# Performance work log

Measured on AMD Instinct MI355X. Metric: run time of the kernel, lower is better.

The kernel has to match this reference:

```python
import jax, jax.numpy as jnp
import numpy as np

N_LIC, N_EMP, N_CON = 40000, 80000, 60000
D_LIC, D_EMP, D_CON = 256, 128, 192
H = 256
E_P, E_Q = 1280000, 640000


def setup_inputs() -> dict:
    key = jax.random.key(0)
    ks = jax.random.split(key, 13)
    s = 0.05
    return {
        "x_lic": jax.random.normal(ks[0], (N_LIC, D_LIC), jnp.float32),
        "x_emp": jax.random.normal(ks[1], (N_EMP, D_EMP), jnp.float32),
        "x_con": jax.random.normal(ks[2], (N_CON, D_CON), jnp.float32),
        "Wl_p": jax.random.normal(ks[3], (D_EMP, H), jnp.float32) * s,
        "Wr_p": jax.random.normal(ks[4], (D_LIC, H), jnp.float32) * s,
        "b_p": jax.random.normal(ks[5], (H,), jnp.float32) * s,
        "Wl_q": jax.random.normal(ks[6], (D_CON, H), jnp.float32) * s,
        "Wr_q": jax.random.normal(ks[7], (D_LIC, H), jnp.float32) * s,
        "b_q": jax.random.normal(ks[8], (H,), jnp.float32) * s,
        "ei_p_src": jax.random.randint(ks[9], (E_P,), 0, N_EMP, jnp.int64),
        "ei_p_dst": jax.random.randint(ks[10], (E_P,), 0, N_LIC, jnp.int64),
        "ei_q_src": jax.random.randint(ks[11], (E_Q,), 0, N_CON, jnp.int64),
        "ei_q_dst": jax.random.randint(ks[12], (E_Q,), 0, N_LIC, jnp.int64),
    }


def _sage_conv(x_src, x_dst, src, dst, Wl, Wr, b):
    """PyG SAGEConv (mean aggr): lin_l(mean_neighbors) + lin_r(x_dst) + bias."""
    n_dst = x_dst.shape[0]
    # gather src features per edge, scatter-sum to dst nodes
    agg = jax.ops.segment_sum(x_src[src], dst, num_segments=n_dst)  # [n_dst, d_src]
    deg = jax.ops.segment_sum(jnp.ones(src.shape, x_src.dtype), dst, num_segments=n_dst)
    agg = agg / jnp.maximum(deg, 1.0)[:, None]  # zero-degree nodes -> 0 (PyG semantics)
    return agg @ Wl + x_dst @ Wr + b


def reference(x_lic, x_emp, x_con, Wl_p, Wr_p, b_p, Wl_q, Wr_q, b_q,
              ei_p_src, ei_p_dst, ei_q_src, ei_q_dst):
    # to_hetero dispatch: two relations target 'licitacion'; aggr='mean' across relations.
    out_p = _sage_conv(x_emp, x_lic, ei_p_src, ei_p_dst, Wl_p, Wr_p, b_p)  # empresa->licitacion
    out_q = _sage_conv(x_con, x_lic, ei_q_src, ei_q_dst, Wl_q, Wr_q, b_q)  # contrato->licitacion
    # forward returns x_dict['licitacion'] after relu; other dst types are dead code.
    return jax.nn.relu(0.5 * (out_p + out_q))
```

## Files before the change

### kernel.cpp

```cpp
#include <hip/hip_runtime.h>

#define N_LIC 40000
#define N_EMP 80000
#define N_CON 60000
#define D_EMP 128
#define D_CON 192
#define HDIM  256
#define E_P   1280000
#define E_Q   640000
#define E_T   (E_P + E_Q)

#define NSEG  64
#define SEGW  (2 * NSEG)
#define SUBR  (N_LIC / NSEG)

#define OFF_AGGP   0
#define OFF_STG    OFF_AGGP
#define OFF_XE     (OFF_AGGP + 2560000)
#define OFF_AGGQ   OFF_XE
#define OFF_XC     (OFF_XE + 5120000)
#define OFF_BPK    (OFF_XC + 5760000)
#define OFF_BIAS   (OFF_BPK + 73728)
#define OFF_CNT    (OFF_BIAS + 256)
#define OFF_SEGT   (OFF_CNT + 2 * N_LIC)
#define OFF_SEGB   (OFF_SEGT + 128)
#define OFF_SEGC   (OFF_SEGB + 128)
#define OFF_OFFP   (OFF_SEGC + 128)
#define OFF_OFFQ   (OFF_OFFP + N_LIC)
#define OFF_SRTP   (OFF_OFFQ + N_LIC)
#define OFF_SRTQ   (OFF_SRTP + E_P)

typedef short bf16x8 __attribute__((ext_vector_type(8)));
typedef float f32x4 __attribute__((ext_vector_type(4)));

__device__ __forceinline__ ushort f2bf(float f) {
    union { float f; uint u; } v; v.f = f;
    return (ushort)((v.u + 0x7fffu + ((v.u >> 16) & 1u)) >> 16);
}

__device__ __forceinline__ void acc2(uint u, float& lo, float& hi) {
    union { uint u; float f; } a, b;
    a.u = u << 16;
    b.u = u & 0xffff0000u;
    lo += a.f; hi += b.f;
}

__device__ __forceinline__ uint packbf(float lo, float hi) {
    return (uint)f2bf(lo) | ((uint)f2bf(hi) << 16);
}

__global__ void prep_kernel(const float* __restrict__ Wlp, const float* __restrict__ Wlq,
                            const float* __restrict__ Wrp, const float* __restrict__ Wrq,
                            const float* __restrict__ bp, const float* __restrict__ bq,
                            ushort* __restrict__ Bpk, float* __restrict__ bias) {
    int tid = blockIdx.x * 256 + threadIdx.x;
    if (tid < 256 * 576) {
        int n = tid / 576, k = tid - n * 576;
        float v;
        if (k < 128)      v = Wlp[k * 256 + n];
        else if (k < 320) v = Wlq[(k - 128) * 256 + n];
        else              v = Wrp[(k - 320) * 256 + n] + Wrq[(k - 320) * 256 + n];
        Bpk[tid] = f2bf(v);
    } else if (tid < 256 * 576 + 256) {
        int j = tid - 256 * 576;
        bias[j] = bp[j] + bq[j];
    }
}

#define C_XE (N_EMP * 128 / 4)
#define C_XC (N_CON * 192 / 4)
__global__ void convert2_kernel(const float* __restrict__ xemp, const float* __restrict__ xcon,
                                ushort* __restrict__ xe, ushort* __restrict__ xc) {
    int tid = blockIdx.x * 256 + threadIdx.x;
    const float* src; ushort* dst; int i;
    if (tid < C_XE) { src = xemp; dst = xe; i = tid; }
    else            { src = xcon; dst = xc; i = tid - C_XE; }
    float4 v = ((const float4*)src)[i];
    uint2 o;
    o.x = packbf(v.x, v.y);
    o.y = packbf(v.z, v.w);
    ((uint2*)dst)[i] = o;
}

__global__ __launch_bounds__(256) void precount_kernel(const int* __restrict__ dp,
                                                       const int* __restrict__ dq,
                                                       int* __restrict__ segtot) {
    __shared__ int lc[SEGW];
    int t = threadIdx.x;
    if (t < SEGW) lc[t] = 0;
    __syncthreads();
    int base = blockIdx.x * 2048 + t;
    #pragma unroll
    for (int i = 0; i < 8; i++) {
        int e = base + i * 256;
        if (e < E_T) {
            int d, rel;
            if (e < E_P) { d = __builtin_nontemporal_load(&dp[e]); rel = 0; }
            else         { d = __builtin_nontemporal_load(&dq[e - E_P]); rel = 1; }
            atomicAdd(&lc[rel * NSEG + d / SUBR], 1);
        }
    }
    __syncthreads();
    if (t < SEGW && lc[t] > 0) atomicAdd(&segtot[t], lc[t]);
}

__global__ void segbase_kernel(const int* __restrict__ segtot,
                               int* __restrict__ segbase, int* __restrict__ segcur) {
    if (threadIdx.x == 0) {
        int run = 0;
        for (int i = 0; i < SEGW; i++) {
            segbase[i] = run; segcur[i] = run;
            run += segtot[i];
        }
    }
}

__global__ __launch_bounds__(256) void partition_kernel(const int* __restrict__ sp,
                                                        const int* __restrict__ dp,
                                                        const int* __restrict__ sq,
                                                        const int* __restrict__ dq,
                                                        int* __restrict__ segcur,
                                                        uint* __restrict__ stg) {
    __shared__ int lc[SEGW], inc[SEGW], lb[SEGW], gb[SEGW];
    __shared__ uint srtd[2048];
    __shared__ uchar sid[2048];
    int t = threadIdx.x;
    if (t < SEGW) lc[t] = 0;
    __syncthreads();
    int seg[8], lo[8]; uint pk[8];
    int base = blockIdx.x * 2048 + t;
    #pragma unroll
    for (int i = 0; i < 8; i++) {
        int e = base + i * 256;
        seg[i] = -1;
        if (e < E_T) {
            int d, s, rel;
            if (e < E_P) {
                d = __builtin_nontemporal_load(&dp[e]);
                s = __builtin_nontemporal_load(&sp[e]); rel = 0;
            } else {
                int eq = e - E_P;
                d = __builtin_nontemporal_load(&dq[eq]);
                s = __builtin_nontemporal_load(&sq[eq]); rel = 1;
            }
            int sl = d / SUBR;
            int dl = d - sl * SUBR;
            seg[i] = rel * NSEG + sl;
            pk[i] = ((uint)dl << 17) | (uint)s;
            lo[i] = atomicAdd(&lc[seg[i]], 1);
        }
    }
    __syncthreads();
    if (t < SEGW) inc[t] = lc[t];
    __syncthreads();
    #pragma unroll
    for (int off = 1; off < SEGW; off <<= 1) {
        int v = (t >= off && t < SEGW) ? inc[t - off] : 0;
        __syncthreads();
        if (t < SEGW) inc[t] += v;
        __syncthreads();
    }
    if (t < SEGW) {
        lb[t] = inc[t] - lc[t];
        gb[t] = lc[t] > 0 ? atomicAdd(&segcur[t], lc[t]) : 0;
    }
    __syncthreads();
    #pragma unroll
    for (int i = 0; i < 8; i++) {
        if (seg[i] >= 0) {
            int p = lb[seg[i]] + lo[i];
            srtd[p] = pk[i];
            sid[p] = (uchar)seg[i];
        }
    }
    __syncthreads();
    int tot = inc[SEGW - 1];
    for (int p = t; p < tot; p += 256) {
        int s = sid[p];
        stg[gb[s] + (p - lb[s])] = srtd[p];
    }
}

#define LCAP 22528
__global__ __launch_bounds__(1024) void sort_kernel(const int* __restrict__ segbase,
                                                    const int* __restrict__ segcur,
                                                    const uint* __restrict__ stg,
                                                    int* __restrict__ srtp, int* __restrict__ srtq,
                                                    int* __restrict__ offp, int* __restrict__ offq,
                                                    int* __restrict__ cnt) {
    __shared__ int lcnt[SUBR], lcur[SUBR];
    __shared__ int sc[640];
    __shared__ uint buf[LCAP];
    int s = blockIdx.x;
    int rel = s >> 6;
    int beg = segbase[s], end = segcur[s];
    int t = threadIdx.x;
    if (t < SUBR) { lcnt[t] = 0; lcur[t] = 0; }
    __syncthreads();
    for (int idx = beg + t; idx < end; idx += 1024)
        atomicAdd(&lcnt[stg[idx] >> 17], 1);
    __syncthreads();
    if (t < 640) sc[t] = (t < SUBR) ? lcnt[t] : 0;
    __syncthreads();
    #pragma unroll
    for (int off = 1; off < 640; off <<= 1) {
        int v = (t >= off && t < 640) ? sc[t - off] : 0;
        __syncthreads();
        if (t < 640) sc[t] += v;
        __syncthreads();
    }
    int rb = (rel == 0) ? beg : beg - E_P;
    int* srt = (rel == 0) ? srtp : srtq;
    for (int idx = beg + t; idx < end; idx += 1024) {
        uint p = stg[idx];
        int dl = (int)(p >> 17);
        int pos = sc[dl] - lcnt[dl] + atomicAdd(&lcur[dl], 1);
        uint sv = p & 0x1FFFFu;
        if (pos < LCAP) buf[pos] = sv;
        else srt[rb + pos] = (int)sv;
    }
    __syncthreads();
    int n = end - beg;
    int m = n < LCAP ? n : LCAP;
    for (int p = t; p < m; p += 1024) srt[rb + p] = (int)buf[p];
    int dbase = (s & (NSEG - 1)) * SUBR;
    int* offs = (rel == 0) ? offp : offq;
    int* cn = (rel == 0) ? cnt : cnt + N_LIC;
    if (t < SUBR) {
        offs[dbase + t] = rb + sc[t] - lcnt[t];
        cn[dbase + t] = lcnt[t];
    }
}

__global__ __launch_bounds__(256) void aggP_kernel(const ushort* __restrict__ xe,
                                                   const int* __restrict__ offs,
                                                   const int* __restrict__ cnt,
                                                   const int* __restrict__ sorted,
                                                   ushort* __restrict__ agg) {
    int g = blockIdx.x * 16 + (threadIdx.x >> 4);
    int c = threadIdx.x & 15;
    int beg = offs[g], deg = cnt[g], end = beg + deg;
    float a0=0,a1=0,a2=0,a3=0,a4=0,a5=0,a6=0,a7=0;
    for (int eb = beg; eb < end; eb += 16) {
        int n = end - eb; if (n > 16) n = 16;
        int my = (c < n) ? sorted[eb + c] : 0;
        for (int j = 0; j < n; j++) {
            int s = __shfl(my, j, 16);
            uint4 v = *(const uint4*)(xe + (size_t)s * D_EMP + c * 8);
            acc2(v.x, a0, a1); acc2(v.y, a2, a3);
            acc2(v.z, a4, a5); acc2(v.w, a6, a7);
        }
    }
    float inv = 1.0f / fmaxf((float)deg, 1.0f);
    uint4 o;
    o.x = packbf(a0 * inv, a1 * inv);
    o.y = packbf(a2 * inv, a3 * inv);
    o.z = packbf(a4 * inv, a5 * inv);
    o.w = packbf(a6 * inv, a7 * inv);
    *(uint4*)(agg + (size_t)g * D_EMP + c * 8) = o;
}

__global__ __launch_bounds__(256) void aggQ_kernel(const ushort* __restrict__ xc,
                                                   const int* __restrict__ offs,
                                                   const int* __restrict__ cnt,
                                                   const int* __restrict__ sorted,
                                                   ushort* __restrict__ agg) {
    int g = blockIdx.x * 16 + (threadIdx.x >> 4);
    int c = threadIdx.x & 15;
    int beg = offs[g], deg = cnt[g], end = beg + deg;
    float a0=0,a1=0,a2=0,a3=0,a4=0,a5=0,a6=0,a7=0,a8=0,a9=0,a10=0,a11=0;
    for (int eb = beg; eb < end; eb += 16) {
        int n = end - eb; if (n > 16) n = 16;
        int my = (c < n) ? sorted[eb + c] : 0;
        for (int j = 0; j < n; j++) {
            int s = __shfl(my, j, 16);
            const ushort* row = xc + (size_t)s * D_CON + c * 12;
            uint2 v0 = *(const uint2*)(row + 0);
            uint2 v1 = *(const uint2*)(row + 4);
            uint2 v2 = *(const uint2*)(row + 8);
            acc2(v0.x, a0, a1);  acc2(v0.y, a2, a3);
            acc2(v1.x, a4, a5);  acc2(v1.y, a6, a7);
            acc2(v2.x, a8, a9);  acc2(v2.y, a10, a11);
        }
    }
    float inv = 1.0f / fmaxf((float)deg, 1.0f);
    ushort* o = agg + (size_t)g * D_CON + c * 12;
    uint2 w0, w1, w2;
    w0.x = packbf(a0 * inv, a1 * inv);   w0.y = packbf(a2 * inv, a3 * inv);
    w1.x = packbf(a4 * inv, a5 * inv);   w1.y = packbf(a6 * inv, a7 * inv);
    w2.x = packbf(a8 * inv, a9 * inv);   w2.y = packbf(a10 * inv, a11 * inv);
    *(uint2*)(o + 0) = w0;
    *(uint2*)(o + 4) = w1;
    *(uint2*)(o + 8) = w2;
}

__global__ __launch_bounds__(256) void gemm_kernel(
    const ushort* __restrict__ aggp, const ushort* __restrict__ aggq,
    const float* __restrict__ xlic, const ushort* __restrict__ Bpk,
    const float* __restrict__ bias, float* __restrict__ out)
{
    const int t = threadIdx.x;
    const int m0 = blockIdx.x * 64;
    const int lane = t & 63;
    const int wave = t >> 6;
    const int l15 = lane & 15;
    const int lh  = lane >> 4;

    f32x4 acc[4][4];
    #pragma unroll
    for (int i = 0; i < 4; i++)
        #pragma unroll
        for (int j = 0; j < 4; j++)
            acc[i][j] = (f32x4){0.f, 0.f, 0.f, 0.f};

    const ushort* Bbase = Bpk + (size_t)(wave * 64 + l15) * 576 + lh * 8;

    for (int k0 = 0; k0 < 576; k0 += 32) {
        bf16x8 af[4], bfr[4];
        #pragma unroll
        for (int nt = 0; nt < 4; nt++)
            bfr[nt] = *(const bf16x8*)(Bbase + (size_t)nt * 16 * 576 + k0);
        if (k0 < 128) {
            #pragma unroll
            for (int mt = 0; mt < 4; mt++)
                af[mt] = *(const bf16x8*)(aggp + (size_t)(m0 + mt * 16 + l15) * 128 + k0 + lh * 8);
        } else if (k0 < 320) {
            #pragma unroll
            for (int mt = 0; mt < 4; mt++)
                af[mt] = *(const bf16x8*)(aggq + (size_t)(m0 + mt * 16 + l15) * 192 + (k0 - 128) + lh * 8);
        } else {
            #pragma unroll
            for (int mt = 0; mt < 4; mt++) {
                const float* src = xlic + (size_t)(m0 + mt * 16 + l15) * 256 + (k0 - 320) + lh * 8;
                float4 v0 = *(const float4*)(src + 0);
                float4 v1 = *(const float4*)(src + 4);
                union { uint4 u; bf16x8 b; } cv;
                cv.u.x = packbf(v0.x, v0.y);
                cv.u.y = packbf(v0.z, v0.w);
                cv.u.z = packbf(v1.x, v1.y);
                cv.u.w = packbf(v1.z, v1.w);
                af[mt] = cv.b;
            }
        }
        #pragma unroll
        for (int mt = 0; mt < 4; mt++)
            #pragma unroll
            for (int nt = 0; nt < 4; nt++)
                acc[mt][nt] = __builtin_amdgcn_mfma_f32_16x16x32_bf16(af[mt], bfr[nt], acc[mt][nt], 0, 0, 0);
    }

    #pragma unroll
    for (int nt = 0; nt < 4; nt++) {
        int n = wave * 64 + nt * 16 + l15;
        float bv = bias[n];
        #pragma unroll
        for (int mt = 0; mt < 4; mt++) {
            #pragma unroll
            for (int r = 0; r < 4; r++) {
                int m = m0 + mt * 16 + lh * 4 + r;
                float v = 0.5f * (acc[mt][nt][r] + bv);
                out[(size_t)m * 256 + n] = fmaxf(v, 0.f);
            }
        }
    }
}

extern "C" void kernel_launch(void* const* d_in, const int* in_sizes, int n_in,
                              void* d_out, int out_size, void* d_ws, size_t ws_size,
                              hipStream_t stream) {
    const float* x_lic = (const float*)d_in[0];
    const float* x_emp = (const float*)d_in[1];
    const float* x_con = (const float*)d_in[2];
    const float* Wl_p  = (const float*)d_in[3];
    const float* Wr_p  = (const float*)d_in[4];
    const float* b_p   = (const float*)d_in[5];
    const float* Wl_q  = (const float*)d_in[6];
    const float* Wr_q  = (const float*)d_in[7];
    const float* b_q   = (const float*)d_in[8];
    const int* ei_p_src = (const int*)d_in[9];
    const int* ei_p_dst = (const int*)d_in[10];
    const int* ei_q_src = (const int*)d_in[11];
    const int* ei_q_dst = (const int*)d_in[12];

    float* ws = (float*)d_ws;
    ushort* aggp = (ushort*)(ws + OFF_AGGP);
    ushort* aggq = (ushort*)(ws + OFF_AGGQ);
    uint*  stg  = (uint*)(ws + OFF_STG);
    ushort* xe   = (ushort*)(ws + OFF_XE);
    ushort* xc   = (ushort*)(ws + OFF_XC);
    ushort* Bpk  = (ushort*)(ws + OFF_BPK);
    float* bias  = ws + OFF_BIAS;
    int* cnt  = (int*)(ws + OFF_CNT);
    int* segt = (int*)(ws + OFF_SEGT);
    int* segb = (int*)(ws + OFF_SEGB);
    int* segc = (int*)(ws + OFF_SEGC);
    int* offp = (int*)(ws + OFF_OFFP);
    int* offq = (int*)(ws + OFF_OFFQ);
    int* srtp = (int*)(ws + OFF_SRTP);
    int* srtq = (int*)(ws + OFF_SRTQ);
    float* out = (float*)d_out;

    hipMemsetAsync(segt, 0, SEGW * sizeof(int), stream);

    prep_kernel<<<(256 * 576 + 256 + 255) / 256, 256, 0, stream>>>(Wl_p, Wl_q, Wr_p, Wr_q, b_p, b_q, Bpk, bias);

    convert2_kernel<<<(C_XE + C_XC) / 256, 256, 0, stream>>>(x_emp, x_con, xe, xc);

    const int NBP = (E_T + 2047) / 2048;
    precount_kernel<<<NBP, 256, 0, stream>>>(ei_p_dst, ei_q_dst, segt);
    segbase_kernel<<<1, 64, 0, stream>>>(segt, segb, segc);
    partition_kernel<<<NBP, 256, 0, stream>>>(ei_p_src, ei_p_dst, ei_q_src, ei_q_dst, segc, stg);

    sort_kernel<<<SEGW, 1024, 0, stream>>>(segb, segc, stg, srtp, srtq, offp, offq, cnt);

    aggP_kernel<<<N_LIC / 16, 256, 0, stream>>>(xe, offp, cnt, srtp, aggp);
    aggQ_kernel<<<N_LIC / 16, 256, 0, stream>>>(xc, offq, cnt + N_LIC, srtq, aggq);

    gemm_kernel<<<N_LIC / 64, 256, 0, stream>>>(aggp, aggq, x_lic, Bpk, bias, out);
}
```

Measured before the change: 408.7 us.

## Stage GEMM tiles through double-buffered LDS with register prefetch

The GEMM kernel now cooperatively loads A and B tiles into padded, double-buffered shared memory, prefetching the next k-slice into registers while MFMAs run on the current buffer. Before, each wave read its fragments straight from global memory, and the four waves fetched the same A rows redundantly. This cuts duplicate global traffic and overlaps loads with compute, at the cost of LDS usage, a barrier per k-step and more register pressure.

```diff
diff --git a/kernel.cpp b/kernel.cpp
--- a/kernel.cpp
+++ b/kernel.cpp
@@ -299,10 +299,15 @@
     const float* __restrict__ xlic, const ushort* __restrict__ Bpk,
     const float* __restrict__ bias, float* __restrict__ out)
 {
+    __shared__ __align__(16) ushort As[2][64 * 40];
+    __shared__ __align__(16) ushort Bs[2][256 * 40];
+
     const int t = threadIdx.x;
     const int m0 = blockIdx.x * 64;
     const int lane = t & 63;
     const int wave = t >> 6;
+    const int arow = t >> 2;
+    const int achk = t & 3;
     const int l15 = lane & 15;
     const int lh  = lane >> 4;
 
@@ -313,41 +318,73 @@
         for (int j = 0; j < 4; j++)
             acc[i][j] = (f32x4){0.f, 0.f, 0.f, 0.f};
 
-    const ushort* Bbase = Bpk + (size_t)(wave * 64 + l15) * 576 + lh * 8;
-
-    for (int k0 = 0; k0 < 576; k0 += 32) {
-        bf16x8 af[4], bfr[4];
-        #pragma unroll
-        for (int nt = 0; nt < 4; nt++)
-            bfr[nt] = *(const bf16x8*)(Bbase + (size_t)nt * 16 * 576 + k0);
-        if (k0 < 128) {
-            #pragma unroll
-            for (int mt = 0; mt < 4; mt++)
-                af[mt] = *(const bf16x8*)(aggp + (size_t)(m0 + mt * 16 + l15) * 128 + k0 + lh * 8);
-        } else if (k0 < 320) {
-            #pragma unroll
-            for (int mt = 0; mt < 4; mt++)
-                af[mt] = *(const bf16x8*)(aggq + (size_t)(m0 + mt * 16 + l15) * 192 + (k0 - 128) + lh * 8);
-        } else {
-            #pragma unroll
-            for (int mt = 0; mt < 4; mt++) {
-                const float* src = xlic + (size_t)(m0 + mt * 16 + l15) * 256 + (k0 - 320) + lh * 8;
-                float4 v0 = *(const float4*)(src + 0);
-                float4 v1 = *(const float4*)(src + 4);
-                union { uint4 u; bf16x8 b; } cv;
-                cv.u.x = packbf(v0.x, v0.y);
-                cv.u.y = packbf(v0.z, v0.w);
-                cv.u.z = packbf(v1.x, v1.y);
-                cv.u.w = packbf(v1.z, v1.w);
-                af[mt] = cv.b;
-            }
-        }
-        #pragma unroll
-        for (int mt = 0; mt < 4; mt++)
-            #pragma unroll
-            for (int nt = 0; nt < 4; nt++)
-                acc[mt][nt] = __builtin_amdgcn_mfma_f32_16x16x32_bf16(af[mt], bfr[nt], acc[mt][nt], 0, 0, 0);
-    }
+    uint4 pb0, pb1, pb2, pb3, pa0, pa1;
+
+    #define REG_LOAD(k0)                                                                     \
+    {                                                                                        \
+        pb0 = *(const uint4*)(Bpk + (size_t)(arow +   0) * 576 + (k0) + achk * 8);           \
+        pb1 = *(const uint4*)(Bpk + (size_t)(arow +  64) * 576 + (k0) + achk * 8);           \
+        pb2 = *(const uint4*)(Bpk + (size_t)(arow + 128) * 576 + (k0) + achk * 8);           \
+        pb3 = *(const uint4*)(Bpk + (size_t)(arow + 192) * 576 + (k0) + achk * 8);           \
+        if ((k0) < 128) {                                                                    \
+            pa0 = *(const uint4*)(aggp + (size_t)(m0 + arow) * 128 + (k0) + achk * 8);       \
+        } else if ((k0) < 320) {                                                             \
+            pa0 = *(const uint4*)(aggq + (size_t)(m0 + arow) * 192 + ((k0) - 128) + achk * 8); \
+        } else {                                                                             \
+            const float* src_ = xlic + (size_t)(m0 + arow) * 256 + ((k0) - 320) + achk * 8;  \
+            pa0 = *(const uint4*)(src_ + 0);                                                 \
+            pa1 = *(const uint4*)(src_ + 4);                                                 \
+        }                                                                                    \
+    }
+
+    #define LDS_WRITE(b, k0)                                                                 \
+    {                                                                                        \
+        uint4 aw;                                                                            \
+        if ((k0) < 320) aw = pa0;                                                            \
+        else {                                                                               \
+            union { uint4 u; float f[4]; } c0, c1;                                           \
+            c0.u = pa0; c1.u = pa1;                                                          \
+            aw.x = packbf(c0.f[0], c0.f[1]);                                                 \
+            aw.y = packbf(c0.f[2], c0.f[3]);                                                 \
+            aw.z = packbf(c1.f[0], c1.f[1]);                                                 \
+            aw.w = packbf(c1.f[2], c1.f[3]);                                                 \
+        }                                                                                    \
+        *(uint4*)(&As[b][arow * 40 + achk * 8]) = aw;                                        \
+        *(uint4*)(&Bs[b][(arow +   0) * 40 + achk * 8]) = pb0;                               \
+        *(uint4*)(&Bs[b][(arow +  64) * 40 + achk * 8]) = pb1;                               \
+        *(uint4*)(&Bs[b][(arow + 128) * 40 + achk * 8]) = pb2;                               \
+        *(uint4*)(&Bs[b][(arow + 192) * 40 + achk * 8]) = pb3;                               \
+    }
+
+    #define COMPUTE(b)                                                                       \
+    {                                                                                        \
+        bf16x8 af[4], bfr[4];                                                                \
+        _Pragma("unroll")                                                                    \
+        for (int mt = 0; mt < 4; mt++)                                                       \
+            af[mt] = *(const bf16x8*)(&As[b][(mt * 16 + l15) * 40 + lh * 8]);                \
+        _Pragma("unroll")                                                                    \
+        for (int nt = 0; nt < 4; nt++)                                                       \
+            bfr[nt] = *(const bf16x8*)(&Bs[b][(wave * 64 + nt * 16 + l15) * 40 + lh * 8]);   \
+        _Pragma("unroll")                                                                    \
+        for (int mt = 0; mt < 4; mt++)                                                       \
+            _Pragma("unroll")                                                                \
+            for (int nt = 0; nt < 4; nt++)                                                   \
+                acc[mt][nt] = __builtin_amdgcn_mfma_f32_16x16x32_bf16(af[mt], bfr[nt], acc[mt][nt], 0, 0, 0); \
+    }
+
+    REG_LOAD(0);
+    LDS_WRITE(0, 0);
+    __syncthreads();
+
+    int cur = 0;
+    for (int k0 = 32; k0 < 576; k0 += 32) {
+        REG_LOAD(k0);
+        COMPUTE(cur);
+        LDS_WRITE(cur ^ 1, k0);
+        __syncthreads();
+        cur ^= 1;
+    }
+    COMPUTE(cur);
 
     #pragma unroll
     for (int nt = 0; nt < 4; nt++) {
@@ -363,6 +400,9 @@
             }
         }
     }
+    #undef REG_LOAD
+    #undef LDS_WRITE
+    #undef COMPUTE
 }
 
 extern "C" void kernel_launch(void* const* d_in, const int* in_sizes, int n_in,
```

Result: faster. 365.7 us (-10.5%).
